# Performance work log

Measured on AMD Instinct MI355X. Metric: run time of the kernel, lower is better.

## Reference

```python
import jax, jax.numpy as jnp
import numpy as np

RANK = 3
NUM_STEPS = 3
NUM_ENT = 40000
NUM_EMB = 24
NUM_OPS = 12
DIM = 128
HID = 128
BATCH = 128
NNZ = 300000


def _lstm_dir(x, Wih, Whh, bih, bhh, reverse=False):
    # x: (S, B, D); PyTorch gate order i, f, g, o
    B = x.shape[1]
    H = Whh.shape[1]
    def step(carry, xt):
        h, c = carry
        z = xt @ Wih.T + h @ Whh.T + bih + bhh  # (B, 4H)
        i, f, g, o = jnp.split(z, 4, axis=-1)
        c = jax.nn.sigmoid(f) * c + jax.nn.sigmoid(i) * jnp.tanh(g)
        h = jax.nn.sigmoid(o) * jnp.tanh(c)
        return (h, c), h
    init = (jnp.zeros((B, H), x.dtype), jnp.zeros((B, H), x.dtype))
    _, hs = jax.lax.scan(step, init, x, reverse=reverse)
    return hs  # (S, B, H)


def _spmm(memory, src, dst, val, num_ent):
    # memory: (B, E); edges (src -> dst): out[b, j] = sum_{e: dst[e]=j} memory[b, src[e]] * val[e]
    g = memory[:, src] * val[None, :]              # (B, nnz)
    out = jax.ops.segment_sum(g.T, dst, num_segments=num_ent)  # (E, B)
    return out.T


def setup_inputs() -> dict:
    key = jax.random.key(0)
    ks = jax.random.split(key, 16)
    inp = {
        'queries': jax.random.randint(ks[0], (BATCH,), 0, NUM_EMB),
        'heads': jax.random.randint(ks[1], (BATCH,), 0, NUM_ENT),
        'edge_src': jax.random.randint(ks[2], (NUM_OPS, NNZ), 0, NUM_ENT, dtype=jnp.int32),
        'edge_dst': jax.random.randint(ks[3], (NUM_OPS, NNZ), 0, NUM_ENT, dtype=jnp.int32),
        'edge_val': jax.random.uniform(ks[4], (NUM_OPS, NNZ), jnp.float32),
        'emb': jax.random.normal(ks[5], (NUM_EMB, DIM), jnp.float32) * 0.1,
        'Wih_f': jax.random.normal(ks[6], (RANK, 4 * HID, DIM), jnp.float32) * 0.1,
        'Whh_f': jax.random.normal(ks[7], (RANK, 4 * HID, HID), jnp.float32) * 0.1,
        'bih_f': jnp.zeros((RANK, 4 * HID), jnp.float32),
        'bhh_f': jnp.zeros((RANK, 4 * HID), jnp.float32),
        'Wih_b': jax.random.normal(ks[8], (RANK, 4 * HID, DIM), jnp.float32) * 0.1,
        'Whh_b': jax.random.normal(ks[9], (RANK, 4 * HID, HID), jnp.float32) * 0.1,
        'bih_b': jnp.zeros((RANK, 4 * HID), jnp.float32),
        'bhh_b': jnp.zeros((RANK, 4 * HID), jnp.float32),
        'W0': jax.random.normal(ks[10], (2 * HID, NUM_OPS + 1), jnp.float32) * 0.1,
        'b0': jnp.zeros((1, NUM_OPS + 1), jnp.float32),
    }
    return inp


def reference(queries, heads, edge_src, edge_dst, edge_val, emb,
              Wih_f, Whh_f, bih_f, bhh_f, Wih_b, Whh_b, bih_b, bhh_b, W0, b0):
    # query embedding replicated over time: (S, B, D)
    q = emb[queries]
    x = jnp.broadcast_to(q[None], (NUM_STEPS, q.shape[0], q.shape[1]))
    head_onehot = jax.nn.one_hot(heads, NUM_ENT, dtype=jnp.float32)  # (B, E)

    logits = jnp.zeros((q.shape[0], NUM_ENT), jnp.float32)
    for r in range(RANK):
        hf = _lstm_dir(x, Wih_f[r], Whh_f[r], bih_f[r], bhh_f[r], reverse=False)
        hb = _lstm_dir(x, Wih_b[r], Whh_b[r], bih_b[r], bhh_b[r], reverse=True)
        rnn_out = jnp.concatenate([hf, hb], axis=-1)          # (S, B, 2H)
        trans = rnn_out @ W0 + b0                             # (S, B, ops+1)
        attn = jax.nn.softmax(trans, axis=-1)
        attn = jnp.transpose(attn, (0, 2, 1))                 # (S, ops+1, B)

        memory = head_onehot                                  # (B, E)
        for t in range(NUM_STEPS):
            attn_t = attn[t]                                  # (ops+1, B)
            acc = memory * attn_t[-1][:, None]                # identity operator
            for op in range(NUM_OPS):
                prod = _spmm(memory, edge_src[op], edge_dst[op], edge_val[op], NUM_ENT)
                acc = acc + prod * attn_t[op][:, None]
            memory = acc
        norm = jnp.maximum(jnp.float32(1e-20), jnp.sum(memory, axis=1, keepdims=True))
        logits = logits + memory / norm
    return logits
```

## Files before the change

kernel.cpp:

```cpp
#include <hip/hip_runtime.h>

#define NENT 40000
#define NB 128
#define NQ 24
#define NOPS 12
#define EPO 300000
#define NTOT (NOPS * EPO)
#define NRANK 3
#define NPASS 8
#define CP 16
#define ECAP 160

typedef float v4f __attribute__((ext_vector_type(4)));

__device__ __forceinline__ v4f shfl_xor4(v4f x, int m) {
    v4f r;
    r.x = __shfl_xor(x.x, m);
    r.y = __shfl_xor(x.y, m);
    r.z = __shfl_xor(x.z, m);
    r.w = __shfl_xor(x.w, m);
    return r;
}

__device__ __forceinline__ bool bittest(const unsigned* bm, int i) {
    return (bm[i >> 5] >> (i & 31)) & 1u;
}

__global__ void headmark_kernel(const int* __restrict__ heads, unsigned* __restrict__ bmH,
                                unsigned* __restrict__ bm2) {
    int h = heads[threadIdx.x];
    atomicOr(&bmH[h >> 5], 1u << (h & 31));
    atomicOr(&bm2[h >> 5], 1u << (h & 31));
}

__global__ void mark2_kernel(const int* __restrict__ src, const int* __restrict__ dst,
                             const unsigned* __restrict__ bmH, unsigned* __restrict__ bm2) {
    int i = blockIdx.x * 256 + threadIdx.x;
    if (i < NTOT) {
        int s = src[i];
        if (bittest(bmH, s)) {
            int d = dst[i];
            atomicOr(&bm2[d >> 5], 1u << (d & 31));
        }
    }
}

__global__ void build_ell_kernel(const int* __restrict__ src, const int* __restrict__ dst,
                                 const float* __restrict__ val, const unsigned* __restrict__ bm2,
                                 int* __restrict__ fillD, int* __restrict__ fillS,
                                 int2* __restrict__ eD, int2* __restrict__ eS) {
    int i = blockIdx.x * 256 + threadIdx.x;
    if (i >= NTOT) return;
    int s = src[i], d = dst[i];
    int op = i / EPO;
    int v = __float_as_int(val[i]);
    int pd = atomicAdd(&fillD[d], 1);
    eD[(size_t)d * ECAP + pd] = make_int2(s | (op << 16), v);
    if (bittest(bm2, s)) {
        int ps = atomicAdd(&fillS[s], 1);
        eS[(size_t)s * ECAP + ps] = make_int2(d | (op << 16), v);
    }
}

__global__ void zxq_kernel(const float* __restrict__ emb,
                           const float* __restrict__ Wih_f, const float* __restrict__ bih_f,
                           const float* __restrict__ bhh_f,
                           const float* __restrict__ Wih_b, const float* __restrict__ bih_b,
                           const float* __restrict__ bhh_b,
                           float* __restrict__ zxq) {
    int combo = blockIdx.x / NQ;
    int q = blockIdx.x % NQ;
    int dir = combo / 3, r = combo % 3;
    const float* Wih = (dir ? Wih_b : Wih_f) + r * 512 * 128;
    const float* bih = (dir ? bih_b : bih_f) + r * 512;
    const float* bhh = (dir ? bhh_b : bhh_f) + r * 512;
    __shared__ float x[128];
    int u = threadIdx.x;
    x[u] = emb[q * 128 + u];
    __syncthreads();
    const float* W0p = Wih + u * 128;
    const float* W1p = Wih + (128 + u) * 128;
    const float* W2p = Wih + (256 + u) * 128;
    const float* W3p = Wih + (384 + u) * 128;
    float a0 = 0.f, a1 = 0.f, a2 = 0.f, a3 = 0.f;
    for (int d = 0; d < 128; ++d) {
        float xv = x[d];
        a0 = fmaf(xv, W0p[d], a0);
        a1 = fmaf(xv, W1p[d], a1);
        a2 = fmaf(xv, W2p[d], a2);
        a3 = fmaf(xv, W3p[d], a3);
    }
    float* o = zxq + (size_t)(combo * NQ + q) * 512;
    o[u]       = a0 + bih[u]       + bhh[u];
    o[128 + u] = a1 + bih[128 + u] + bhh[128 + u];
    o[256 + u] = a2 + bih[256 + u] + bhh[256 + u];
    o[384 + u] = a3 + bih[384 + u] + bhh[384 + u];
}

__global__ void lstmq_kernel(const float* __restrict__ Whh_f, const float* __restrict__ Whh_b,
                             const float* __restrict__ zxq, float* __restrict__ hq) {
    int combo = blockIdx.x / NQ;
    int q = blockIdx.x % NQ;
    int dir = combo / 3, r = combo % 3;
    const float* Whh = (dir ? Whh_b : Whh_f) + r * 512 * 128;
    __shared__ float h[128];
    int u = threadIdx.x;
    const float* z = zxq + (size_t)(combo * NQ + q) * 512;
    float zi0 = z[u], zf0 = z[128 + u], zg0 = z[256 + u], zo0 = z[384 + u];
    const float* Wi = Whh + u * 128;
    const float* Wf = Whh + (128 + u) * 128;
    const float* Wg = Whh + (256 + u) * 128;
    const float* Wo = Whh + (384 + u) * 128;
    float c = 0.f;
    h[u] = 0.f;
    for (int s = 0; s < 3; ++s) {
        __syncthreads();
        float a0 = 0.f, a1 = 0.f, a2 = 0.f, a3 = 0.f;
        for (int d = 0; d < 128; ++d) {
            float hv = h[d];
            a0 = fmaf(hv, Wi[d], a0);
            a1 = fmaf(hv, Wf[d], a1);
            a2 = fmaf(hv, Wg[d], a2);
            a3 = fmaf(hv, Wo[d], a3);
        }
        float ig = 1.f / (1.f + expf(-(zi0 + a0)));
        float fg = 1.f / (1.f + expf(-(zf0 + a1)));
        float gg = tanhf(zg0 + a2);
        float og = 1.f / (1.f + expf(-(zo0 + a3)));
        c = fg * c + ig * gg;
        float hn = og * tanhf(c);
        __syncthreads();
        h[u] = hn;
        hq[(size_t)((combo * 3 + s) * NQ + q) * 128 + u] = hn;
    }
}

__global__ void attnq_kernel(const float* __restrict__ hq, const float* __restrict__ W0,
                             const float* __restrict__ b0, float* __restrict__ attnq) {
    int r = blockIdx.x / 3, t = blockIdx.x % 3;
    __shared__ float W0s[256 * 13];
    for (int idx = threadIdx.x; idx < 256 * 13; idx += 32) W0s[idx] = W0[idx];
    __syncthreads();
    int q = threadIdx.x;
    if (q >= NQ) return;
    float acc[13];
    for (int k = 0; k < 13; ++k) acc[k] = b0[k];
    const float* hf = hq + (size_t)(((0 * 3 + r) * 3 + t) * NQ + q) * 128;
    const float* hb = hq + (size_t)(((1 * 3 + r) * 3 + (2 - t)) * NQ + q) * 128;
    for (int u = 0; u < 128; ++u) {
        float v = hf[u];
        for (int k = 0; k < 13; ++k) acc[k] = fmaf(v, W0s[u * 13 + k], acc[k]);
    }
    for (int u = 0; u < 128; ++u) {
        float v = hb[u];
        for (int k = 0; k < 13; ++k) acc[k] = fmaf(v, W0s[(128 + u) * 13 + k], acc[k]);
    }
    float m = acc[0];
    for (int k = 1; k < 13; ++k) m = fmaxf(m, acc[k]);
    float e[13];
    float sum = 0.f;
    for (int k = 0; k < 13; ++k) { e[k] = expf(acc[k] - m); sum += e[k]; }
    float inv = 1.f / sum;
    float* ao = attnq + (size_t)(r * 3 + t) * 13 * NQ;
    for (int k = 0; k < 13; ++k) ao[k * NQ + q] = e[k] * inv;
}

__global__ void expand_kernel(const int* __restrict__ queries, const float* __restrict__ attnq,
                              float* __restrict__ attn) {
    __shared__ int qs[128];
    if (threadIdx.x < 128) qs[threadIdx.x] = queries[threadIdx.x];
    __syncthreads();
    for (int idx = threadIdx.x; idx < 9 * 13 * 128; idx += 256) {
        int b = idx & 127, kk = idx >> 7;
        attn[idx] = attnq[kk * NQ + qs[b]];
    }
}

__global__ void fused01_kernel(const int* __restrict__ heads, const float* __restrict__ attn,
                               const int* __restrict__ fillS, const int2* __restrict__ eS,
                               float* __restrict__ mem2) {
    int r = blockIdx.y;
    int b = blockIdx.x;
    __shared__ float c0s[13], c1s[13];
    if (threadIdx.x < 13) {
        c0s[threadIdx.x] = attn[(size_t)((r * 3 + 0) * 13 + threadIdx.x) * 128 + b];
        c1s[threadIdx.x] = attn[(size_t)((r * 3 + 1) * 13 + threadIdx.x) * 128 + b];
    }
    __syncthreads();
    int h = heads[b];
    int lenH = fillS[h];
    float* mem = mem2 + ((size_t)(r * NPASS + (b >> 4)) * NENT) * CP + (b & 15);
    for (int ent = threadIdx.x; ent < lenH + 1; ent += 128) {
        int i; float wv;
        if (ent == 0) { i = h; wv = c0s[12]; }
        else {
            int2 e = eS[(size_t)h * ECAP + ent - 1];
            i = e.x & 0xFFFF;
            wv = __int_as_float(e.y) * c0s[e.x >> 16];
        }
        atomicAdd(&mem[(size_t)i * CP], c1s[12] * wv);
        int lenI = fillS[i];
        const int2* ei = eS + (size_t)i * ECAP;
        for (int f = 0; f < lenI; ++f) {
            int2 e2 = ei[f];
            atomicAdd(&mem[(size_t)(e2.x & 0xFFFF) * CP],
                      __int_as_float(e2.y) * c1s[e2.x >> 16] * wv);
        }
    }
}

__global__ __launch_bounds__(256) void dense_kernel(const float* __restrict__ attn,
                                                    const int* __restrict__ fillD,
                                                    const int2* __restrict__ edgesD,
                                                    const float* __restrict__ in,
                                                    float* __restrict__ out,
                                                    float* __restrict__ normv) {
    int p = blockIdx.x;
    int r = blockIdx.z;
    __shared__ __align__(16) float cs[13 * 20];
    __shared__ float npart[4][16];
    int tid = threadIdx.x;
    if (tid < 13 * 16) {
        int op = tid >> 4, c0 = tid & 15;
        cs[op * 20 + c0] = attn[(size_t)((r * 3 + 2) * 13 + op) * 128 + p * CP + c0];
    }
    __syncthreads();
    int wave = tid >> 6, lane = tid & 63;
    int slot = lane >> 2;
    int cq4 = (lane & 3) * 4;
    int jw = blockIdx.y * 16 + wave * 4;
    const float* inr = in + (size_t)(r * NPASS + p) * NENT * CP;
    float* outr = out + (size_t)(r * NPASS + p) * NENT * CP;
    int lens[4];
    const int2* edp[4];
#pragma unroll
    for (int t = 0; t < 4; ++t) {
        lens[t] = fillD[jw + t];
        edp[t] = edgesD + (size_t)(jw + t) * ECAP;
    }
    int maxlen = max(max(lens[0], lens[1]), max(lens[2], lens[3]));
    v4f acc[4];
#pragma unroll
    for (int t = 0; t < 4; ++t) acc[t] = (v4f)0.f;

    for (int base = 0; base < maxlen; base += 32) {
        int2 e[8];
        bool m[8];
#pragma unroll
        for (int t = 0; t < 4; ++t) {
            int ia = base + slot;
            int ib = base + 16 + slot;
            m[t]     = ia < lens[t];
            m[4 + t] = ib < lens[t];
            e[t]     = edp[t][m[t] ? ia : 0];
            e[4 + t] = edp[t][m[4 + t] ? ib : 0];
        }
        v4f g[8];
#pragma unroll
        for (int u = 0; u < 8; ++u)
            g[u] = *(const v4f*)(inr + (size_t)(e[u].x & 0xFFFF) * CP + cq4);
#pragma unroll
        for (int u = 0; u < 8; ++u) {
            v4f cc = *(const v4f*)&cs[(e[u].x >> 16) * 20 + cq4];
            float v = m[u] ? __int_as_float(e[u].y) : 0.f;
            acc[u & 3] += (v * cc) * g[u];
        }
    }

    v4f cid = *(const v4f*)&cs[12 * 20 + cq4];
    v4f rsum = (v4f)0.f;
#pragma unroll
    for (int t = 0; t < 4; ++t) {
        v4f red = acc[t];
        red += shfl_xor4(red, 4);
        red += shfl_xor4(red, 8);
        red += shfl_xor4(red, 16);
        red += shfl_xor4(red, 32);
        if (slot == 0) {
            int j = jw + t;
            v4f mi = *(const v4f*)(inr + (size_t)j * CP + cq4);
            v4f res = cid * mi + red;
            *(v4f*)(outr + (size_t)j * CP + cq4) = res;
            rsum += res;
        }
    }
    if (slot == 0) *(v4f*)&npart[wave][cq4] = rsum;
    __syncthreads();
    if (tid < 16) {
        float s = npart[0][tid] + npart[1][tid] + npart[2][tid] + npart[3][tid];
        atomicAdd(&normv[r * 128 + p * CP + tid], s);
    }
}

__global__ void rnorm_kernel(const float* __restrict__ normv, float* __restrict__ rnormv) {
    int i = threadIdx.x;
    rnormv[i] = 1.f / fmaxf(normv[i], 1e-20f);
}

__global__ void final_kernel(const float* __restrict__ mem3, const float* __restrict__ rnormv,
                             float* __restrict__ out) {
    __shared__ float tile[32 * 129];
    __shared__ float rn[384];
    for (int idx = threadIdx.x; idx < 384; idx += 256) rn[idx] = rnormv[idx];
    __syncthreads();
    int j0 = blockIdx.x * 32;
    for (int p = 0; p < NPASS; ++p) {
        for (int it = 0; it < 2; ++it) {
            int lin = it * 256 + threadIdx.x;
            int jj = lin >> 4, c = lin & 15;
            int b = p * CP + c;
            float s = 0.f;
            for (int r = 0; r < 3; ++r)
                s += mem3[((size_t)(r * NPASS + p) * NENT + j0 + jj) * CP + c] * rn[r * 128 + b];
            tile[jj * 129 + b] = s;
        }
    }
    __syncthreads();
    for (int it = 0; it < 16; ++it) {
        int lin = it * 256 + threadIdx.x;
        int b = lin >> 5, jj = lin & 31;
        out[(size_t)b * NENT + j0 + jj] = tile[jj * 129 + b];
    }
}

extern "C" void kernel_launch(void* const* d_in, const int* in_sizes, int n_in,
                              void* d_out, int out_size, void* d_ws, size_t ws_size,
                              hipStream_t stream) {
    const int*   queries  = (const int*)d_in[0];
    const int*   heads    = (const int*)d_in[1];
    const int*   edge_src = (const int*)d_in[2];
    const int*   edge_dst = (const int*)d_in[3];
    const float* edge_val = (const float*)d_in[4];
    const float* emb      = (const float*)d_in[5];
    const float* Wih_f    = (const float*)d_in[6];
    const float* Whh_f    = (const float*)d_in[7];
    const float* bih_f    = (const float*)d_in[8];
    const float* bhh_f    = (const float*)d_in[9];
    const float* Wih_b    = (const float*)d_in[10];
    const float* Whh_b    = (const float*)d_in[11];
    const float* bih_b    = (const float*)d_in[12];
    const float* bhh_b    = (const float*)d_in[13];
    const float* W0       = (const float*)d_in[14];
    const float* b0       = (const float*)d_in[15];
    float* out = (float*)d_out;

    char* w = (char*)d_ws;
    size_t off = 0;
    auto alloc = [&](size_t bytes) -> void* {
        off = (off + 255) & ~(size_t)255;
        void* p = w + off;
        off += bytes;
        return p;
    };
    float* attnq  = (float*)alloc((size_t)9 * 13 * NQ * sizeof(float));
    float* attn   = (float*)alloc((size_t)9 * 13 * 128 * sizeof(float));
    float* zxq    = (float*)alloc((size_t)6 * NQ * 512 * sizeof(float));
    float* hq     = (float*)alloc((size_t)6 * 3 * NQ * 128 * sizeof(float));
    unsigned* bmH = (unsigned*)alloc((2 * 1250 + 2 * NENT) * sizeof(int));
    unsigned* bm2 = bmH + 1250;
    int* fillD    = (int*)(bm2 + 1250);
    int* fillS    = fillD + NENT;
    int2*  eD     = (int2*)alloc((size_t)NENT * ECAP * sizeof(int2));
    float* mem2   = (float*)alloc((size_t)NRANK * NENT * NB * sizeof(float));
    float* mem3   = (float*)alloc((size_t)NRANK * NENT * NB * sizeof(float));
    int2*  eS     = (int2*)mem3;
    float* normv  = (float*)alloc((size_t)NRANK * NB * sizeof(float));
    float* rnormv = (float*)alloc((size_t)NRANK * NB * sizeof(float));

    int cooGrid = (NTOT + 255) / 256;

    hipMemsetAsync(bmH, 0, (2 * 1250 + 2 * NENT) * sizeof(int), stream);
    headmark_kernel<<<1, 128, 0, stream>>>(heads, bmH, bm2);
    mark2_kernel<<<cooGrid, 256, 0, stream>>>(edge_src, edge_dst, bmH, bm2);
    build_ell_kernel<<<cooGrid, 256, 0, stream>>>(edge_src, edge_dst, edge_val, bm2,
                                                  fillD, fillS, eD, eS);

    zxq_kernel<<<6 * NQ, 128, 0, stream>>>(emb, Wih_f, bih_f, bhh_f, Wih_b, bih_b, bhh_b, zxq);
    lstmq_kernel<<<6 * NQ, 128, 0, stream>>>(Whh_f, Whh_b, zxq, hq);
    attnq_kernel<<<9, 32, 0, stream>>>(hq, W0, b0, attnq);
    expand_kernel<<<1, 256, 0, stream>>>(queries, attnq, attn);

    hipMemsetAsync(mem2, 0, (size_t)NRANK * NENT * NB * sizeof(float), stream);
    hipMemsetAsync(normv, 0, NRANK * NB * sizeof(float), stream);
    {
        dim3 g(NB, NRANK);
        fused01_kernel<<<g, 128, 0, stream>>>(heads, attn, fillS, eS, mem2);
    }
    {
        dim3 g(NPASS, NENT / 16, NRANK);
        dense_kernel<<<g, 256, 0, stream>>>(attn, fillD, eD, mem2, mem3, normv);
    }

    rnorm_kernel<<<1, NRANK * NB, 0, stream>>>(normv, rnormv);
    final_kernel<<<NENT / 32, 256, 0, stream>>>(mem3, rnormv, out);
}
```

Baseline: 1.289 ms.

## Fuse small LSTM/attention kernels and parallelize two-hop scatter across lanes

Merges the input-projection and recurrent LSTM kernels into one, folds the attention expand step into its consumers through direct query indexing, and folds the reciprocal-norm kernel into the final kernel. This removes several tiny launches and their intermediate buffers. fused01 now splits each head's neighbor list over 2 z-chunks, and 8 lanes cooperate on each second-hop edge list, which adds parallelism to the atomic scatter. The trade-off is more blocks doing atomics at the same time, which may raise contention.

```diff
diff --git a/kernel.cpp b/kernel.cpp
--- a/kernel.cpp
+++ b/kernel.cpp
@@ -62,19 +62,22 @@
     }
 }
 
-__global__ void zxq_kernel(const float* __restrict__ emb,
-                           const float* __restrict__ Wih_f, const float* __restrict__ bih_f,
-                           const float* __restrict__ bhh_f,
-                           const float* __restrict__ Wih_b, const float* __restrict__ bih_b,
-                           const float* __restrict__ bhh_b,
-                           float* __restrict__ zxq) {
+__global__ void lstm_all_kernel(const float* __restrict__ emb,
+                                const float* __restrict__ Wih_f, const float* __restrict__ bih_f,
+                                const float* __restrict__ bhh_f,
+                                const float* __restrict__ Wih_b, const float* __restrict__ bih_b,
+                                const float* __restrict__ bhh_b,
+                                const float* __restrict__ Whh_f, const float* __restrict__ Whh_b,
+                                float* __restrict__ hq) {
     int combo = blockIdx.x / NQ;
     int q = blockIdx.x % NQ;
     int dir = combo / 3, r = combo % 3;
     const float* Wih = (dir ? Wih_b : Wih_f) + r * 512 * 128;
     const float* bih = (dir ? bih_b : bih_f) + r * 512;
     const float* bhh = (dir ? bhh_b : bhh_f) + r * 512;
+    const float* Whh = (dir ? Whh_b : Whh_f) + r * 512 * 128;
     __shared__ float x[128];
+    __shared__ float h[128];
     int u = threadIdx.x;
     x[u] = emb[q * 128 + u];
     __syncthreads();
@@ -90,23 +93,10 @@
         a2 = fmaf(xv, W2p[d], a2);
         a3 = fmaf(xv, W3p[d], a3);
     }
-    float* o = zxq + (size_t)(combo * NQ + q) * 512;
-    o[u]       = a0 + bih[u]       + bhh[u];
-    o[128 + u] = a1 + bih[128 + u] + bhh[128 + u];
-    o[256 + u] = a2 + bih[256 + u] + bhh[256 + u];
-    o[384 + u] = a3 + bih[384 + u] + bhh[384 + u];
-}
-
-__global__ void lstmq_kernel(const float* __restrict__ Whh_f, const float* __restrict__ Whh_b,
-                             const float* __restrict__ zxq, float* __restrict__ hq) {
-    int combo = blockIdx.x / NQ;
-    int q = blockIdx.x % NQ;
-    int dir = combo / 3, r = combo % 3;
-    const float* Whh = (dir ? Whh_b : Whh_f) + r * 512 * 128;
-    __shared__ float h[128];
-    int u = threadIdx.x;
-    const float* z = zxq + (size_t)(combo * NQ + q) * 512;
-    float zi0 = z[u], zf0 = z[128 + u], zg0 = z[256 + u], zo0 = z[384 + u];
+    float zi0 = a0 + bih[u]       + bhh[u];
+    float zf0 = a1 + bih[128 + u] + bhh[128 + u];
+    float zg0 = a2 + bih[256 + u] + bhh[256 + u];
+    float zo0 = a3 + bih[384 + u] + bhh[384 + u];
     const float* Wi = Whh + u * 128;
     const float* Wf = Whh + (128 + u) * 128;
     const float* Wg = Whh + (256 + u) * 128;
@@ -115,18 +105,18 @@
     h[u] = 0.f;
     for (int s = 0; s < 3; ++s) {
         __syncthreads();
-        float a0 = 0.f, a1 = 0.f, a2 = 0.f, a3 = 0.f;
+        float b0 = 0.f, b1 = 0.f, b2 = 0.f, b3 = 0.f;
         for (int d = 0; d < 128; ++d) {
             float hv = h[d];
-            a0 = fmaf(hv, Wi[d], a0);
-            a1 = fmaf(hv, Wf[d], a1);
-            a2 = fmaf(hv, Wg[d], a2);
-            a3 = fmaf(hv, Wo[d], a3);
-        }
-        float ig = 1.f / (1.f + expf(-(zi0 + a0)));
-        float fg = 1.f / (1.f + expf(-(zf0 + a1)));
-        float gg = tanhf(zg0 + a2);
-        float og = 1.f / (1.f + expf(-(zo0 + a3)));
+            b0 = fmaf(hv, Wi[d], b0);
+            b1 = fmaf(hv, Wf[d], b1);
+            b2 = fmaf(hv, Wg[d], b2);
+            b3 = fmaf(hv, Wo[d], b3);
+        }
+        float ig = 1.f / (1.f + expf(-(zi0 + b0)));
+        float fg = 1.f / (1.f + expf(-(zf0 + b1)));
+        float gg = tanhf(zg0 + b2);
+        float og = 1.f / (1.f + expf(-(zo0 + b3)));
         c = fg * c + ig * gg;
         float hn = og * tanhf(c);
         __syncthreads();
@@ -139,7 +129,7 @@
                              const float* __restrict__ b0, float* __restrict__ attnq) {
     int r = blockIdx.x / 3, t = blockIdx.x % 3;
     __shared__ float W0s[256 * 13];
-    for (int idx = threadIdx.x; idx < 256 * 13; idx += 32) W0s[idx] = W0[idx];
+    for (int idx = threadIdx.x; idx < 256 * 13; idx += 128) W0s[idx] = W0[idx];
     __syncthreads();
     int q = threadIdx.x;
     if (q >= NQ) return;
@@ -165,32 +155,25 @@
     for (int k = 0; k < 13; ++k) ao[k * NQ + q] = e[k] * inv;
 }
 
-__global__ void expand_kernel(const int* __restrict__ queries, const float* __restrict__ attnq,
-                              float* __restrict__ attn) {
-    __shared__ int qs[128];
-    if (threadIdx.x < 128) qs[threadIdx.x] = queries[threadIdx.x];
-    __syncthreads();
-    for (int idx = threadIdx.x; idx < 9 * 13 * 128; idx += 256) {
-        int b = idx & 127, kk = idx >> 7;
-        attn[idx] = attnq[kk * NQ + qs[b]];
-    }
-}
-
-__global__ void fused01_kernel(const int* __restrict__ heads, const float* __restrict__ attn,
+__global__ void fused01_kernel(const int* __restrict__ heads, const int* __restrict__ queries,
+                               const float* __restrict__ attnq,
                                const int* __restrict__ fillS, const int2* __restrict__ eS,
                                float* __restrict__ mem2) {
     int r = blockIdx.y;
     int b = blockIdx.x;
+    int chunk = blockIdx.z;
     __shared__ float c0s[13], c1s[13];
     if (threadIdx.x < 13) {
-        c0s[threadIdx.x] = attn[(size_t)((r * 3 + 0) * 13 + threadIdx.x) * 128 + b];
-        c1s[threadIdx.x] = attn[(size_t)((r * 3 + 1) * 13 + threadIdx.x) * 128 + b];
+        int qb = queries[b];
+        c0s[threadIdx.x] = attnq[(size_t)((r * 3 + 0) * 13 + threadIdx.x) * NQ + qb];
+        c1s[threadIdx.x] = attnq[(size_t)((r * 3 + 1) * 13 + threadIdx.x) * NQ + qb];
     }
     __syncthreads();
     int h = heads[b];
     int lenH = fillS[h];
     float* mem = mem2 + ((size_t)(r * NPASS + (b >> 4)) * NENT) * CP + (b & 15);
-    for (int ent = threadIdx.x; ent < lenH + 1; ent += 128) {
+    int g = threadIdx.x >> 3, lane8 = threadIdx.x & 7;
+    for (int ent = g + chunk * 32; ent < lenH + 1; ent += 64) {
         int i; float wv;
         if (ent == 0) { i = h; wv = c0s[12]; }
         else {
@@ -198,10 +181,10 @@
             i = e.x & 0xFFFF;
             wv = __int_as_float(e.y) * c0s[e.x >> 16];
         }
-        atomicAdd(&mem[(size_t)i * CP], c1s[12] * wv);
+        if (lane8 == 0) atomicAdd(&mem[(size_t)i * CP], c1s[12] * wv);
         int lenI = fillS[i];
         const int2* ei = eS + (size_t)i * ECAP;
-        for (int f = 0; f < lenI; ++f) {
+        for (int f = lane8; f < lenI; f += 8) {
             int2 e2 = ei[f];
             atomicAdd(&mem[(size_t)(e2.x & 0xFFFF) * CP],
                       __int_as_float(e2.y) * c1s[e2.x >> 16] * wv);
@@ -209,7 +192,8 @@
     }
 }
 
-__global__ __launch_bounds__(256) void dense_kernel(const float* __restrict__ attn,
+__global__ __launch_bounds__(256) void dense_kernel(const int* __restrict__ queries,
+                                                    const float* __restrict__ attnq,
                                                     const int* __restrict__ fillD,
                                                     const int2* __restrict__ edgesD,
                                                     const float* __restrict__ in,
@@ -222,7 +206,7 @@
     int tid = threadIdx.x;
     if (tid < 13 * 16) {
         int op = tid >> 4, c0 = tid & 15;
-        cs[op * 20 + c0] = attn[(size_t)((r * 3 + 2) * 13 + op) * 128 + p * CP + c0];
+        cs[op * 20 + c0] = attnq[(size_t)((r * 3 + 2) * 13 + op) * NQ + queries[p * CP + c0]];
     }
     __syncthreads();
     int wave = tid >> 6, lane = tid & 63;
@@ -292,16 +276,12 @@
     }
 }
 
-__global__ void rnorm_kernel(const float* __restrict__ normv, float* __restrict__ rnormv) {
-    int i = threadIdx.x;
-    rnormv[i] = 1.f / fmaxf(normv[i], 1e-20f);
-}
-
-__global__ void final_kernel(const float* __restrict__ mem3, const float* __restrict__ rnormv,
+__global__ void final_kernel(const float* __restrict__ mem3, const float* __restrict__ normv,
                              float* __restrict__ out) {
     __shared__ float tile[32 * 129];
     __shared__ float rn[384];
-    for (int idx = threadIdx.x; idx < 384; idx += 256) rn[idx] = rnormv[idx];
+    for (int idx = threadIdx.x; idx < 384; idx += 256)
+        rn[idx] = 1.f / fmaxf(normv[idx], 1e-20f);
     __syncthreads();
     int j0 = blockIdx.x * 32;
     for (int p = 0; p < NPASS; ++p) {
@@ -353,8 +333,6 @@
         return p;
     };
     float* attnq  = (float*)alloc((size_t)9 * 13 * NQ * sizeof(float));
-    float* attn   = (float*)alloc((size_t)9 * 13 * 128 * sizeof(float));
-    float* zxq    = (float*)alloc((size_t)6 * NQ * 512 * sizeof(float));
     float* hq     = (float*)alloc((size_t)6 * 3 * NQ * 128 * sizeof(float));
     unsigned* bmH = (unsigned*)alloc((2 * 1250 + 2 * NENT) * sizeof(int));
     unsigned* bm2 = bmH + 1250;
@@ -365,7 +343,6 @@
     float* mem3   = (float*)alloc((size_t)NRANK * NENT * NB * sizeof(float));
     int2*  eS     = (int2*)mem3;
     float* normv  = (float*)alloc((size_t)NRANK * NB * sizeof(float));
-    float* rnormv = (float*)alloc((size_t)NRANK * NB * sizeof(float));
 
     int cooGrid = (NTOT + 255) / 256;
 
@@ -375,22 +352,20 @@
     build_ell_kernel<<<cooGrid, 256, 0, stream>>>(edge_src, edge_dst, edge_val, bm2,
                                                   fillD, fillS, eD, eS);
 
-    zxq_kernel<<<6 * NQ, 128, 0, stream>>>(emb, Wih_f, bih_f, bhh_f, Wih_b, bih_b, bhh_b, zxq);
-    lstmq_kernel<<<6 * NQ, 128, 0, stream>>>(Whh_f, Whh_b, zxq, hq);
-    attnq_kernel<<<9, 32, 0, stream>>>(hq, W0, b0, attnq);
-    expand_kernel<<<1, 256, 0, stream>>>(queries, attnq, attn);
+    lstm_all_kernel<<<6 * NQ, 128, 0, stream>>>(emb, Wih_f, bih_f, bhh_f,
+                                                Wih_b, bih_b, bhh_b, Whh_f, Whh_b, hq);
+    attnq_kernel<<<9, 128, 0, stream>>>(hq, W0, b0, attnq);
 
     hipMemsetAsync(mem2, 0, (size_t)NRANK * NENT * NB * sizeof(float), stream);
     hipMemsetAsync(normv, 0, NRANK * NB * sizeof(float), stream);
     {
-        dim3 g(NB, NRANK);
-        fused01_kernel<<<g, 128, 0, stream>>>(heads, attn, fillS, eS, mem2);
+        dim3 g(NB, NRANK, 2);
+        fused01_kernel<<<g, 256, 0, stream>>>(heads, queries, attnq, fillS, eS, mem2);
     }
     {
         dim3 g(NPASS, NENT / 16, NRANK);
-        dense_kernel<<<g, 256, 0, stream>>>(attn, fillD, eD, mem2, mem3, normv);
-    }
-
-    rnorm_kernel<<<1, NRANK * NB, 0, stream>>>(normv, rnormv);
-    final_kernel<<<NENT / 32, 256, 0, stream>>>(mem3, rnormv, out);
-}
+        dense_kernel<<<g, 256, 0, stream>>>(queries, attnq, fillD, eD, mem2, mem3, normv);
+    }
+
+    final_kernel<<<NENT / 32, 256, 0, stream>>>(mem3, normv, out);
+}
```

New measurement: 1.294 ms. No clear change (+0.4%).
